# Kernel tuning notes

Hardware: AMD Instinct MI355X
Metric: run time of the kernel (lower is better)

Reference implementation:

```python
import jax, jax.numpy as jnp
import numpy as np
import math

B, S, D = 4, 4096, 1024
H = 16
HD = D // H          # head_dim = 64
M = 256              # nb_features (random projection dim)


def _orthogonal_gaussian(key, m, d):
    # FAVOR+ orthogonal random features: blocks of d orthogonal rows,
    # each row rescaled to a chi-distributed norm (norm of a d-dim gaussian).
    n_blocks = int(math.ceil(m / d))
    keys = jax.random.split(key, n_blocks + 1)
    blocks = []
    for i in range(n_blocks):
        g = jax.random.normal(keys[i], (d, d), dtype=jnp.float32)
        q, _ = jnp.linalg.qr(g)
        blocks.append(q.T)
    W = jnp.concatenate(blocks, axis=0)[:m]  # [m, d]
    norms = jnp.linalg.norm(
        jax.random.normal(keys[-1], (m, d), dtype=jnp.float32), axis=1, keepdims=True)
    return W * norms


def _softmax_kernel(x, proj, is_query, eps=1e-4):
    # x: [b,h,s,d]; proj: [m,d]. Standard FAVOR+ positive softmax features.
    d = x.shape[-1]
    ratio = proj.shape[0] ** -0.5
    x = x * (d ** -0.25)
    u = jnp.einsum('bhsd,md->bhsm', x, proj)  # projection
    diag = 0.5 * jnp.sum(x * x, axis=-1, keepdims=True)  # [b,h,s,1]
    if is_query:
        stab = jnp.max(u, axis=-1, keepdims=True)
    else:
        stab = jnp.max(u, axis=(-1, -2), keepdims=True)
    return ratio * (jnp.exp(u - diag - stab) + eps)


def performer_attention(Q, K, V, mask, proj):
    # Q,K,V: [b,h,s,d], mask: [b,s]
    scale = HD ** -0.25
    m4 = mask[:, None, :, None]
    Qs = Q * scale
    Ks = K * scale * m4
    Vs = V * m4
    q_prime = _softmax_kernel(Qs, proj, is_query=True)   # [b,h,s,m]
    k_prime = _softmax_kernel(Ks, proj, is_query=False)  # [b,h,s,m]
    # linear attention: O(s*m*d)
    kv = jnp.einsum('bhsm,bhsd->bhmd', k_prime, Vs)      # [b,h,m,d]
    z = 1.0 / (jnp.einsum('bhsm,bhm->bhs', q_prime, jnp.sum(k_prime, axis=2)) + 1e-6)
    out = jnp.einsum('bhsm,bhmd->bhsd', q_prime, kv) * z[..., None]
    return out


def setup_inputs() -> dict:
    key = jax.random.key(0)
    ks = jax.random.split(key, 9)
    X = jax.random.normal(ks[0], (B, S, D), dtype=jnp.float32)
    mask = jnp.ones((B, S), dtype=jnp.float32)
    s = D ** -0.5
    Wq = jax.random.normal(ks[1], (D, D), dtype=jnp.float32) * s
    bq = jnp.zeros((D,), dtype=jnp.float32)
    Wk = jax.random.normal(ks[2], (D, D), dtype=jnp.float32) * s
    bk = jnp.zeros((D,), dtype=jnp.float32)
    Wv = jax.random.normal(ks[3], (D, D), dtype=jnp.float32) * s
    bv = jnp.zeros((D,), dtype=jnp.float32)
    proj = _orthogonal_gaussian(ks[4], M, HD)
    return {"X": X, "mask": mask, "Wq": Wq, "bq": bq, "Wk": Wk, "bk": bk,
            "Wv": Wv, "bv": bv, "proj": proj}


def _split_heads(x):
    b, s, _ = x.shape
    return x.reshape(b, s, H, HD).transpose(0, 2, 1, 3)


def reference(X, mask, Wq, bq, Wk, bk, Wv, bv, proj):
    Q = _split_heads(X @ Wq + bq)
    K = _split_heads(X @ Wk + bk)
    V = _split_heads(X @ Wv + bv)
    attn = performer_attention(Q, K, V, mask, proj)  # [b,h,s,hd]
    out = attn.transpose(0, 2, 1, 3).reshape(B, S, D)
    return out
```

## Files before the change

### kernel.cpp

```cpp
#include <hip/hip_runtime.h>
#include <stdint.h>

#define DEVI static __device__ __forceinline__

typedef unsigned short u16;
typedef unsigned int u32;
typedef __attribute__((ext_vector_type(8))) short short8;
typedef __attribute__((ext_vector_type(4))) float f32x4;
typedef __attribute__((ext_vector_type(4))) unsigned short ushort4_t;

#define BB 4
#define SS 4096
#define DD 1024
#define HH 16
#define HDD 64
#define MM 256
#define BHN 64

DEVI u16 f2bf(float f) {
    u32 u = __float_as_uint(f);
    u += 0x7fffu + ((u >> 16) & 1u);
    return (u16)(u >> 16);
}
DEVI float bf2f(u16 h) { return __uint_as_float(((u32)h) << 16); }

typedef __attribute__((address_space(1))) const unsigned int as1_u32;
typedef __attribute__((address_space(3))) unsigned int as3_u32;
DEVI void load_lds16(const void* g, void* lds) {
    __builtin_amdgcn_global_load_lds((as1_u32*)g, (as3_u32*)lds, 16, 0, 0);
}


__global__ void conv_bf16(const float* __restrict__ src, u16* __restrict__ dst, int n4) {
    int i = blockIdx.x * 256 + threadIdx.x;
    if (i < n4) {
        float4 v = reinterpret_cast<const float4*>(src)[i];
        ushort4_t o = { f2bf(v.x), f2bf(v.y), f2bf(v.z), f2bf(v.w) };
        reinterpret_cast<ushort4_t*>(dst)[i] = o;
    }
}

__global__ void conv_w(const float* __restrict__ Wq, const float* __restrict__ Wk,
                       const float* __restrict__ Wv, u16* __restrict__ Wt) {
    __shared__ float tile[64][65];
    const int jt = blockIdx.x, kt = blockIdx.y;
    const float* src = (jt < 16) ? Wq : (jt < 32) ? Wk : Wv;
    const int j0 = (jt & 15) * 64, k0 = kt * 64;
    const int t = threadIdx.x;
    for (int i = 0; i < 16; ++i) {
        int lin = t + i * 256;
        int kl = lin >> 6, jl = lin & 63;
        tile[kl][jl] = src[(size_t)(k0 + kl) * DD + j0 + jl];
    }
    __syncthreads();
    const int jg0 = jt * 64;
    for (int i = 0; i < 16; ++i) {
        int lin = t + i * 256;
        int jl = lin >> 6, kl = lin & 63;
        Wt[(size_t)(jg0 + jl) * DD + k0 + kl] = f2bf(tile[kl][jl]);
    }
}

__global__ __launch_bounds__(512, 2) void gemm1_m8(
    const u16* __restrict__ Xbf, const u16* __restrict__ Wt,
    const float* __restrict__ bq, const float* __restrict__ bk, const float* __restrict__ bv,
    const float* __restrict__ mask,
    u16* __restrict__ Qh, u16* __restrict__ Kh, u16* __restrict__ Vt,
    float* __restrict__ dq, float* __restrict__ dk)
{
    extern __shared__ __align__(16) char smem[];
    const int tid = threadIdx.x, l = tid & 63, wv = tid >> 6;
    const int wm = wv >> 2, wn = wv & 3;
    const int bid = blockIdx.x;
    const int xcd = bid & 7, i6 = bid >> 3;
    const int bx = xcd * 8 + i6 / 12, by = i6 % 12;
    const int row0 = bx * 256, col0 = by * 256;

    const int srow = tid >> 3;
    const int scol = ((tid & 7) ^ (srow & 7)) * 8;

    #define ABUF(p) ((char*)smem + (p) * 32768)
    #define BBUF(p) ((char*)smem + 65536 + (p) * 32768)
    #define STA(p, kt, r) load_lds16(Xbf + (size_t)(row0 + (r)*64 + srow) * DD + (kt)*64 + scol, \
                                     ABUF(p) + (r)*8192 + wv*1024)
    #define STB(p, kt, r) load_lds16(Wt + (size_t)(col0 + (r)*64 + srow) * DD + (kt)*64 + scol, \
                                     BBUF(p) + (r)*8192 + wv*1024)

    STA(0,0,0); STA(0,0,1); STA(0,0,2); STA(0,0,3);
    STB(0,0,0); STB(0,0,1); STB(0,0,2); STB(0,0,3);
    STA(1,1,0); STA(1,1,1); STA(1,1,2); STA(1,1,3);
    asm volatile("s_waitcnt vmcnt(4)" ::: "memory");
    __builtin_amdgcn_s_barrier();
    __builtin_amdgcn_sched_barrier(0);

    f32x4 acc[8][4] = {};
    const int arow_b = wm * 128 + (l & 15);
    const int brow_b = wn * 64 + (l & 15);
    const int cb_b = (l >> 4) * 16;
    const int lx = (l & 7) << 4;

    for (int kt = 0; kt < 16; ++kt) {
        const int p = kt & 1, pn = p ^ 1;
        const bool haveN = (kt + 1) < 16;
        short8 bfr[2][2];
#pragma unroll
        for (int ph = 0; ph < 4; ++ph) {
            const int mh = ph & 1, nh = ph >> 1;
            if (haveN) STB(pn, kt + 1, ph);
            if (mh == 0) {
#pragma unroll
                for (int j = 0; j < 2; ++j) {
                    const int br = brow_b + (nh * 2 + j) * 16;
#pragma unroll
                    for (int ks = 0; ks < 2; ++ks)
                        bfr[j][ks] = *(const short8*)(BBUF(p) + br * 128 + ((cb_b + ks * 64) ^ lx));
                }
            }
            short8 a[4][2];
#pragma unroll
            for (int i = 0; i < 4; ++i) {
                const int ar = arow_b + (mh * 4 + i) * 16;
#pragma unroll
                for (int ks = 0; ks < 2; ++ks)
                    a[i][ks] = *(const short8*)(ABUF(p) + ar * 128 + ((cb_b + ks * 64) ^ lx));
            }
            __builtin_amdgcn_s_barrier();
            asm volatile("s_waitcnt lgkmcnt(0)" ::: "memory");
            __builtin_amdgcn_sched_barrier(0);
            __builtin_amdgcn_s_setprio(1);
#pragma unroll
            for (int i = 0; i < 4; ++i)
#pragma unroll
                for (int j = 0; j < 2; ++j) {
                    acc[mh*4+i][nh*2+j] = __builtin_amdgcn_mfma_f32_16x16x32_bf16(a[i][0], bfr[j][0], acc[mh*4+i][nh*2+j], 0, 0, 0);
                    acc[mh*4+i][nh*2+j] = __builtin_amdgcn_mfma_f32_16x16x32_bf16(a[i][1], bfr[j][1], acc[mh*4+i][nh*2+j], 0, 0, 0);
                }
            __builtin_amdgcn_s_setprio(0);
            __builtin_amdgcn_sched_barrier(0);
            __builtin_amdgcn_s_barrier();
        }
        if (kt + 2 < 16) {
            STA(p, kt + 2, 0); STA(p, kt + 2, 1); STA(p, kt + 2, 2); STA(p, kt + 2, 3);
            asm volatile("s_waitcnt vmcnt(4)" ::: "memory");
        } else {
            asm volatile("s_waitcnt vmcnt(0)" ::: "memory");
        }
        __builtin_amdgcn_s_barrier();
        __builtin_amdgcn_sched_barrier(0);
    }

    const int region = by >> 2;
    const int h = ((by & 3) << 2) + wn;
    const int rg = row0 + wm * 128;
    const int b = rg >> 12;
    const int sb = rg & 4095;
    const size_t bh = (size_t)(b * HH + h);
    const int dd = l & 15;
    const int jbase = ((by & 3) << 8) + wn * 64;

    if (region == 0) {
        float bias[4];
#pragma unroll
        for (int nf = 0; nf < 4; ++nf) bias[nf] = bq[jbase + nf * 16 + dd];
#pragma unroll
        for (int mf = 0; mf < 8; ++mf) {
            float ds4[4];
#pragma unroll
            for (int g = 0; g < 4; ++g) {
                const int s = sb + mf * 16 + ((l >> 4) << 2) + g;
                float dsum = 0.f;
#pragma unroll
                for (int nf = 0; nf < 4; ++nf) {
                    u16 hv = f2bf((acc[mf][nf][g] + bias[nf]) * 0.125f);
                    Qh[(bh * SS + s) * HDD + nf * 16 + dd] = hv;
                    float fv = bf2f(hv);
                    dsum += fv * fv;
                }
                dsum += __shfl_xor(dsum, 1);
                dsum += __shfl_xor(dsum, 2);
                dsum += __shfl_xor(dsum, 4);
                dsum += __shfl_xor(dsum, 8);
                ds4[g] = 0.5f * dsum;
            }
            if (dd == 0)
                *(float4*)(dq + bh * SS + sb + mf * 16 + ((l >> 4) << 2)) =
                    make_float4(ds4[0], ds4[1], ds4[2], ds4[3]);
        }
    } else if (region == 1) {
        float bias[4];
#pragma unroll
        for (int nf = 0; nf < 4; ++nf) bias[nf] = bk[jbase + nf * 16 + dd];
#pragma unroll
        for (int mf = 0; mf < 8; ++mf) {
            float ds4[4];
#pragma unroll
            for (int g = 0; g < 4; ++g) {
                const int s = sb + mf * 16 + ((l >> 4) << 2) + g;
                const float m = mask[b * SS + s];
                float dsum = 0.f;
#pragma unroll
                for (int nf = 0; nf < 4; ++nf) {
                    u16 hv = f2bf((acc[mf][nf][g] + bias[nf]) * m * 0.125f);
                    Kh[(bh * SS + s) * HDD + nf * 16 + dd] = hv;
                    float fv = bf2f(hv);
                    dsum += fv * fv;
                }
                dsum += __shfl_xor(dsum, 1);
                dsum += __shfl_xor(dsum, 2);
                dsum += __shfl_xor(dsum, 4);
                dsum += __shfl_xor(dsum, 8);
                ds4[g] = 0.5f * dsum;
            }
            if (dd == 0)
                *(float4*)(dk + bh * SS + sb + mf * 16 + ((l >> 4) << 2)) =
                    make_float4(ds4[0], ds4[1], ds4[2], ds4[3]);
        }
    } else {
        float bias[4];
#pragma unroll
        for (int nf = 0; nf < 4; ++nf) bias[nf] = bv[jbase + nf * 16 + dd];
#pragma unroll
        for (int mf = 0; mf < 8; ++mf) {
            const int s0 = sb + mf * 16 + ((l >> 4) << 2);
#pragma unroll
            for (int nf = 0; nf < 4; ++nf) {
                ushort4_t pk;
#pragma unroll
                for (int g = 0; g < 4; ++g) {
                    const float m = mask[b * SS + s0 + g];
                    pk[g] = f2bf((acc[mf][nf][g] + bias[nf]) * m);
                }
                *(ushort4_t*)(Vt + (bh * HDD + nf * 16 + dd) * SS + s0) = pk;
            }
        }
    }
    #undef ABUF
    #undef BBUF
    #undef STA
    #undef STB
}

__global__ __launch_bounds__(256, 2) void kv_fused(
    const u16* __restrict__ Kh, const u16* __restrict__ Vt,
    const u16* __restrict__ projb, const float* __restrict__ dk,
    float* __restrict__ kv_part, float* __restrict__ ksum_part,
    float* __restrict__ vsum_part, float* __restrict__ lstab)
{
    extern __shared__ __align__(16) char ksm[];
    #define KLDS(b) ((char*)ksm + (b) * 8192)
    #define VLDS(b) ((char*)ksm + 24576 + (b) * 8192)
    u16* Kp = (u16*)((char*)ksm + 49152);
    const int tid = threadIdx.x, l = tid & 63, wv = tid >> 6;
    const int ck = blockIdx.x, bh = blockIdx.y;
    short8 pb[4][2];
#pragma unroll
    for (int nf = 0; nf < 4; ++nf)
#pragma unroll
        for (int ks = 0; ks < 2; ++ks)
            pb[nf][ks] = *(const short8*)(projb + (wv * 64 + nf * 16 + (l & 15)) * HDD + ks * 32 + (l >> 4) * 8);
    const size_t sbase = (size_t)bh * SS + ck * 512;

    #define KSTAGE(buf, it8) do { \
        const int s0_ = (it8) * 64; \
        _Pragma("unroll") \
        for (int c = 0; c < 2; ++c) { \
            const int rb = wv * 16 + c * 8; \
            const int r = rb + (l >> 3); \
            const int sc = ((l & 7) ^ (r & 7)) * 8; \
            load_lds16(Kh + (sbase + s0_ + r) * HDD + sc, KLDS(buf) + rb * 128); \
        } \
    } while (0)
    #define VSTAGE(buf, it8) do { \
        const int s0_ = (it8) * 64; \
        _Pragma("unroll") \
        for (int c = 0; c < 2; ++c) { \
            const int rb = wv * 16 + c * 8; \
            const int r = rb + (l >> 3); \
            const int sc = ((l & 7) ^ (r & 7)) * 8; \
            load_lds16(Vt + ((size_t)bh * HDD + r) * SS + ck * 512 + s0_ + sc, VLDS(buf) + rb * 128); \
        } \
    } while (0)

    float mrun = -3.0e38f;
    f32x4 acc[4][4] = {};
    float ksc[4] = {0.f, 0.f, 0.f, 0.f};
    float vsc[4] = {0.f, 0.f, 0.f, 0.f};
    KSTAGE(0, 0); VSTAGE(0, 0);
    for (int it = 0; it < 8; ++it) {
        if (it + 1 < 8) {
            KSTAGE((it + 1) % 3, it + 1);
            VSTAGE((it + 1) % 3, it + 1);
            asm volatile("s_waitcnt vmcnt(4)" ::: "memory");
        } else {
            asm volatile("s_waitcnt vmcnt(0)" ::: "memory");
        }
        __syncthreads();
        const int bs = it % 3;
        const int s0 = it * 64;
        f32x4 u4[4][4];
#pragma unroll
        for (int sf = 0; sf < 4; ++sf) {
#pragma unroll
            for (int nf = 0; nf < 4; ++nf) u4[sf][nf] = (f32x4){0.f, 0.f, 0.f, 0.f};
            const int s = sf * 16 + (l & 15);
#pragma unroll
            for (int ks = 0; ks < 2; ++ks) {
                short8 ak = *(const short8*)(KLDS(bs) + s * 128 + ((ks * 64 + (l >> 4) * 16) ^ ((s & 7) << 4)));
#pragma unroll
                for (int nf = 0; nf < 4; ++nf)
                    u4[sf][nf] = __builtin_amdgcn_mfma_f32_16x16x32_bf16(ak, pb[nf][ks], u4[sf][nf], 0, 0, 0);
            }
        }
        float pmax = -3.0e38f;
#pragma unroll
        for (int sf = 0; sf < 4; ++sf)
#pragma unroll
            for (int nf = 0; nf < 4; ++nf)
#pragma unroll
                for (int g = 0; g < 4; ++g) pmax = fmaxf(pmax, u4[sf][nf][g]);
#pragma unroll
        for (int o = 1; o < 64; o <<= 1) pmax = fmaxf(pmax, __shfl_xor(pmax, o));
        if (pmax > mrun) {
            const float fac = __expf(mrun - pmax);
            mrun = pmax;
#pragma unroll
            for (int mf = 0; mf < 4; ++mf)
#pragma unroll
                for (int nf = 0; nf < 4; ++nf)
#pragma unroll
                    for (int g = 0; g < 4; ++g) acc[mf][nf][g] *= fac;
#pragma unroll
            for (int nf = 0; nf < 4; ++nf) ksc[nf] *= fac;
        }
#pragma unroll
        for (int sf = 0; sf < 4; ++sf) {
            const int srow = sf * 16 + (l >> 4) * 4;
            const float4 dkv = *(const float4*)(dk + sbase + s0 + srow);
#pragma unroll
            for (int nf = 0; nf < 4; ++nf) {
                const int m = wv * 64 + nf * 16 + (l & 15);
                u16 h0 = f2bf(__expf(u4[sf][nf][0] - dkv.x - mrun));
                u16 h1 = f2bf(__expf(u4[sf][nf][1] - dkv.y - mrun));
                u16 h2 = f2bf(__expf(u4[sf][nf][2] - dkv.z - mrun));
                u16 h3 = f2bf(__expf(u4[sf][nf][3] - dkv.w - mrun));
                ksc[nf] += bf2f(h0) + bf2f(h1) + bf2f(h2) + bf2f(h3);
                uint2 w; w.x = (u32)h0 | ((u32)h1 << 16); w.y = (u32)h2 | ((u32)h3 << 16);
                *(uint2*)((char*)Kp + m * 128 + ((srow * 2) ^ ((m & 7) << 4))) = w;
            }
        }
        __syncthreads();
#pragma unroll
        for (int ks = 0; ks < 2; ++ks) {
            short8 am[4], bv8[4];
#pragma unroll
            for (int mf = 0; mf < 4; ++mf) {
                const int m = wv * 64 + mf * 16 + (l & 15);
                am[mf] = *(const short8*)((const char*)Kp + m * 128 + ((ks * 64 + (l >> 4) * 16) ^ ((m & 7) << 4)));
            }
#pragma unroll
            for (int nf = 0; nf < 4; ++nf) {
                const int d = nf * 16 + (l & 15);
                bv8[nf] = *(const short8*)(VLDS(bs) + d * 128 + ((ks * 64 + (l >> 4) * 16) ^ ((d & 7) << 4)));
                float vs = 0.f;
#pragma unroll
                for (int e = 0; e < 8; ++e) vs += bf2f((u16)bv8[nf][e]);
                vsc[nf] += vs;
            }
#pragma unroll
            for (int mf = 0; mf < 4; ++mf)
#pragma unroll
                for (int nf = 0; nf < 4; ++nf)
                    acc[mf][nf] = __builtin_amdgcn_mfma_f32_16x16x32_bf16(am[mf], bv8[nf], acc[mf][nf], 0, 0, 0);
        }
    }
    if (l == 0) lstab[((size_t)ck * BHN + bh) * 4 + wv] = mrun;
    const size_t pbase = (size_t)ck * BHN + bh;
#pragma unroll
    for (int nf = 0; nf < 4; ++nf) {
        float v = ksc[nf];
        v += __shfl_xor(v, 16);
        v += __shfl_xor(v, 32);
        if (l < 16) ksum_part[pbase * MM + wv * 64 + nf * 16 + l] = v;
        float w = vsc[nf];
        w += __shfl_xor(w, 16);
        w += __shfl_xor(w, 32);
        if (wv == 0 && l < 16) vsum_part[pbase * HDD + nf * 16 + l] = w;
    }
#pragma unroll
    for (int mf = 0; mf < 4; ++mf)
#pragma unroll
        for (int nf = 0; nf < 4; ++nf)
            *(f32x4*)(kv_part + (pbase * HDD + nf * 16 + (l & 15)) * MM + wv * 64 + mf * 16 + (l >> 4) * 4) = acc[mf][nf];
    #undef KLDS
    #undef VLDS
    #undef KSTAGE
    #undef VSTAGE
}

__global__ void reduceB3(const float* __restrict__ kv_part, const float* __restrict__ ksum_part,
                         const float* __restrict__ vsum_part, const float* __restrict__ lstab,
                         u16* __restrict__ Bmat) {
    __shared__ float f[8][4];
    const int bh = blockIdx.x, n = blockIdx.y, t = threadIdx.x;
    if (t < 32) {
        float lv = lstab[((size_t)(t >> 2) * BHN + bh) * 4 + (t & 3)];
        float g = lv;
#pragma unroll
        for (int o = 1; o < 32; o <<= 1) g = fmaxf(g, __shfl_xor(g, o));
        f[t >> 2][t & 3] = __expf(lv - g);
    }
    __syncthreads();
    const int grp = t >> 6;
    float s = 0.f;
    if (n < 64) {
        float vsg = 0.f;
#pragma unroll
        for (int ck = 0; ck < 8; ++ck) {
            vsg += vsum_part[((size_t)ck * BHN + bh) * HDD + n];
            s += kv_part[(((size_t)ck * BHN + bh) * HDD + n) * MM + t] * f[ck][grp];
        }
        s = 0.0625f * (s + 1e-4f * vsg);
    } else if (n == 64) {
#pragma unroll
        for (int ck = 0; ck < 8; ++ck)
            s += ksum_part[((size_t)ck * BHN + bh) * MM + t] * f[ck][grp];
        s = 0.0625f * (s + 1e-4f * 4096.0f);
    }
    Bmat[((size_t)bh * 80 + n) * MM + t] = (n <= 64) ? f2bf(s) : (u16)0;
}

__global__ __launch_bounds__(256) void out_fused(
    const u16* __restrict__ Qh, const u16* __restrict__ projb,
    const float* __restrict__ dq, const u16* __restrict__ Bmat,
    float* __restrict__ out)
{
    __shared__ __align__(16) u16 Qlds[64 * 64];
    __shared__ __align__(16) u16 qlds[64 * 256];
    __shared__ float red[4][64];
    const int tid = threadIdx.x, l = tid & 63, wv = tid >> 6;
    const int rt = blockIdx.x, bh = blockIdx.y;
    const size_t srowbase = (size_t)bh * SS + rt * 64;
#pragma unroll
    for (int c = 0; c < 2; ++c) {
        const int rb = wv * 16 + c * 8;
        const int r = rb + (l >> 3);
        load_lds16(Qh + (srowbase + r) * HDD + (((l & 7) ^ (r & 7)) * 8), (char*)Qlds + rb * 128);
    }
    short8 pa[4][2];
#pragma unroll
    for (int mf = 0; mf < 4; ++mf)
#pragma unroll
        for (int ks = 0; ks < 2; ++ks)
            pa[mf][ks] = *(const short8*)(projb + (wv * 64 + mf * 16 + (l & 15)) * HDD + ks * 32 + (l >> 4) * 8);
    __syncthreads();
    f32x4 u[4][4] = {};
#pragma unroll
    for (int ks = 0; ks < 2; ++ks) {
        short8 bq8[4];
#pragma unroll
        for (int nf = 0; nf < 4; ++nf) {
            const int s = nf * 16 + (l & 15);
            bq8[nf] = *(const short8*)((const char*)Qlds + s * 128 + ((ks * 64 + (l >> 4) * 16) ^ ((s & 7) << 4)));
        }
#pragma unroll
        for (int mf = 0; mf < 4; ++mf)
#pragma unroll
            for (int nf = 0; nf < 4; ++nf)
                u[mf][nf] = __builtin_amdgcn_mfma_f32_16x16x32_bf16(pa[mf][ks], bq8[nf], u[mf][nf], 0, 0, 0);
    }
#pragma unroll
    for (int nf = 0; nf < 4; ++nf) {
        float v = -3.0e38f;
#pragma unroll
        for (int mf = 0; mf < 4; ++mf)
#pragma unroll
            for (int g = 0; g < 4; ++g) v = fmaxf(v, u[mf][nf][g]);
        v = fmaxf(v, __shfl_xor(v, 16));
        v = fmaxf(v, __shfl_xor(v, 32));
        if ((l >> 4) == 0) red[wv][nf * 16 + l] = v;
    }
    __syncthreads();
#pragma unroll
    for (int nf = 0; nf < 4; ++nf) {
        const int s = nf * 16 + (l & 15);
        const float mx = fmaxf(fmaxf(red[0][s], red[1][s]), fmaxf(red[2][s], red[3][s]));
        const float dg = dq[srowbase + s];
#pragma unroll
        for (int mf = 0; mf < 4; ++mf) {
            u16 h0 = f2bf(0.0625f * (__expf(u[mf][nf][0] - dg - mx) + 1e-4f));
            u16 h1 = f2bf(0.0625f * (__expf(u[mf][nf][1] - dg - mx) + 1e-4f));
            u16 h2 = f2bf(0.0625f * (__expf(u[mf][nf][2] - dg - mx) + 1e-4f));
            u16 h3 = f2bf(0.0625f * (__expf(u[mf][nf][3] - dg - mx) + 1e-4f));
            uint2 w; w.x = (u32)h0 | ((u32)h1 << 16); w.y = (u32)h2 | ((u32)h3 << 16);
            const int mb = (wv * 64 + mf * 16 + (l >> 4) * 4) * 2;
            *(uint2*)((char*)qlds + s * 512 + (mb ^ ((s & 7) << 4))) = w;
        }
    }
    __syncthreads();
    const u16* bbase = Bmat + (size_t)bh * 20480;
    f32x4 acc[4][2] = {};
#pragma unroll
    for (int kt = 0; kt < 8; ++kt) {
        short8 aq[4], bb[2];
#pragma unroll
        for (int mf = 0; mf < 4; ++mf) {
            const int s = mf * 16 + (l & 15);
            aq[mf] = *(const short8*)((const char*)qlds + s * 512 + ((kt * 64 + (l >> 4) * 16) ^ ((s & 7) << 4)));
        }
        bb[0] = *(const short8*)(bbase + (wv * 16 + (l & 15)) * 256 + kt * 32 + (l >> 4) * 8);
        bb[1] = *(const short8*)(bbase + (64 + (l & 15)) * 256 + kt * 32 + (l >> 4) * 8);
#pragma unroll
        for (int mf = 0; mf < 4; ++mf)
#pragma unroll
            for (int nf = 0; nf < 2; ++nf)
                acc[mf][nf] = __builtin_amdgcn_mfma_f32_16x16x32_bf16(aq[mf], bb[nf], acc[mf][nf], 0, 0, 0);
    }
    const int b = bh >> 4, h = bh & 15;
#pragma unroll
    for (int mf = 0; mf < 4; ++mf) {
#pragma unroll
        for (int g = 0; g < 4; ++g) {
            const float den = __shfl(acc[mf][1][g], (l & 48));
            const float z = 1.0f / (den + 1e-6f);
            const int s = rt * 64 + mf * 16 + (l >> 4) * 4 + g;
            out[((size_t)b * SS + s) * DD + h * HDD + wv * 16 + (l & 15)] = acc[mf][0][g] * z;
        }
    }
}

extern "C" void kernel_launch(void* const* d_in, const int* in_sizes, int n_in,
                              void* d_out, int out_size, void* d_ws, size_t ws_size,
                              hipStream_t stream)
{
    const float* X    = (const float*)d_in[0];
    const float* mask = (const float*)d_in[1];
    const float* Wq   = (const float*)d_in[2];
    const float* bq   = (const float*)d_in[3];
    const float* Wk   = (const float*)d_in[4];
    const float* bk   = (const float*)d_in[5];
    const float* Wv   = (const float*)d_in[6];
    const float* bv   = (const float*)d_in[7];
    const float* proj = (const float*)d_in[8];
    float* out = (float*)d_out;

    char* p = (char*)d_ws;
    u16* Xbf = (u16*)p;
    float* kv_part = (float*)p; p += 33554432;
    u16* Wt = (u16*)p;    p += 6291456;
    u16* projb = (u16*)p; p += 32768;
    u16* Qh = (u16*)p;    p += 33554432;
    u16* Kh = (u16*)p;    p += 33554432;
    u16* Vt = (u16*)p;    p += 33554432;
    float* dq = (float*)p; p += 1048576;
    float* dk = (float*)p; p += 1048576;
    float* ksum_part = (float*)p; p += 524288;
    u16* Bmat = (u16*)p;  p += 2621440;
    float* vsum_part = (float*)p; p += 131072;
    float* lstab = (float*)p; p += 8192;
    if (ws_size < 145924096ull) return;

    hipFuncSetAttribute((const void*)gemm1_m8, hipFuncAttributeMaxDynamicSharedMemorySize, 131072);
    hipFuncSetAttribute((const void*)kv_fused, hipFuncAttributeMaxDynamicSharedMemorySize, 81920);

    conv_bf16<<<16384, 256, 0, stream>>>(X, Xbf, 4194304);
    conv_w<<<dim3(48, 16), 256, 0, stream>>>(Wq, Wk, Wv, Wt);
    conv_bf16<<<16, 256, 0, stream>>>(proj, projb, 4096);
    gemm1_m8<<<768, 512, 131072, stream>>>(Xbf, Wt, bq, bk, bv, mask, Qh, Kh, Vt, dq, dk);
    kv_fused<<<dim3(8, 64), 256, 81920, stream>>>(Kh, Vt, projb, dk, kv_part, ksum_part, vsum_part, lstab);
    reduceB3<<<dim3(64, 80), 256, 0, stream>>>(kv_part, ksum_part, vsum_part, lstab, Bmat);
    out_fused<<<dim3(64, 64), 256, 0, stream>>>(Qh, projb, dq, Bmat, out);
}
```

Measured before the change: 268.8 us.

## Halve GEMM K-tile to 32 with new LDS swizzle to double occupancy

Reworks the QKV projection GEMM to use a K step of 32 instead of 64, halving the LDS footprint from 128KB to 64KB and raising the launch bound to allow more resident blocks. The LDS layout and swizzle are redone so two 32-wide rows share a 128-byte line, and the pipeline becomes a simple double buffer with one barrier per K step instead of per-phase barriers. This is meant to improve latency hiding through occupancy, at the cost of twice as many loop iterations and waiting on all loads each step (vmcnt(0)). With 512 threads and 128 accumulator floats per thread, register pressure may cap actual occupancy.

```diff
diff --git a/kernel.cpp b/kernel.cpp
--- a/kernel.cpp
+++ b/kernel.cpp
@@ -61,7 +61,7 @@
     }
 }
 
-__global__ __launch_bounds__(512, 2) void gemm1_m8(
+__global__ __launch_bounds__(512, 4) void gemm1_bk32(
     const u16* __restrict__ Xbf, const u16* __restrict__ Wt,
     const float* __restrict__ bq, const float* __restrict__ bk, const float* __restrict__ bv,
     const float* __restrict__ mask,
@@ -76,75 +76,66 @@
     const int bx = xcd * 8 + i6 / 12, by = i6 % 12;
     const int row0 = bx * 256, col0 = by * 256;
 
-    const int srow = tid >> 3;
-    const int scol = ((tid & 7) ^ (srow & 7)) * 8;
-
-    #define ABUF(p) ((char*)smem + (p) * 32768)
-    #define BBUF(p) ((char*)smem + 65536 + (p) * 32768)
-    #define STA(p, kt, r) load_lds16(Xbf + (size_t)(row0 + (r)*64 + srow) * DD + (kt)*64 + scol, \
-                                     ABUF(p) + (r)*8192 + wv*1024)
-    #define STB(p, kt, r) load_lds16(Wt + (size_t)(col0 + (r)*64 + srow) * DD + (kt)*64 + scol, \
-                                     BBUF(p) + (r)*8192 + wv*1024)
-
-    STA(0,0,0); STA(0,0,1); STA(0,0,2); STA(0,0,3);
-    STB(0,0,0); STB(0,0,1); STB(0,0,2); STB(0,0,3);
-    STA(1,1,0); STA(1,1,1); STA(1,1,2); STA(1,1,3);
-    asm volatile("s_waitcnt vmcnt(4)" ::: "memory");
+    int sA[2];
+#pragma unroll
+    for (int j = 0; j < 2; ++j) {
+        const int o = j * 8192 + tid * 16;
+        const int R = o >> 7;
+        const int logpos = (o & 127) ^ ((R & 7) << 4);
+        const int r = 2 * R + (logpos >> 6);
+        const int c8 = (logpos >> 4) & 3;
+        sA[j] = r * DD + c8 * 8;
+    }
+    const size_t xbase = (size_t)row0 * DD;
+    const size_t wbase = (size_t)col0 * DD;
+
+    #define ABUF(b) ((char*)smem + (b) * 16384)
+    #define BBUF(b) ((char*)smem + 32768 + (b) * 16384)
+    #define STA(b, kt, j) load_lds16(Xbf + xbase + (kt) * 32 + sA[j], ABUF(b) + (j) * 8192 + wv * 1024)
+    #define STB(b, kt, j) load_lds16(Wt + wbase + (kt) * 32 + sA[j], BBUF(b) + (j) * 8192 + wv * 1024)
+
+    STA(0, 0, 0); STA(0, 0, 1); STB(0, 0, 0); STB(0, 0, 1);
+    asm volatile("s_waitcnt vmcnt(0)" ::: "memory");
     __builtin_amdgcn_s_barrier();
     __builtin_amdgcn_sched_barrier(0);
 
     f32x4 acc[8][4] = {};
-    const int arow_b = wm * 128 + (l & 15);
-    const int brow_b = wn * 64 + (l & 15);
-    const int cb_b = (l >> 4) * 16;
-    const int lx = (l & 7) << 4;
-
-    for (int kt = 0; kt < 16; ++kt) {
+    const int hl = (l & 15) >> 1;
+    const int xorc = hl << 4;
+    const int pa = ((wm * 64 + hl) * 128 + (l & 1) * 64 + (l >> 4) * 16) ^ xorc;
+    const int pb = ((wn * 32 + hl) * 128 + (l & 1) * 64 + (l >> 4) * 16) ^ xorc;
+
+    for (int kt = 0; kt < 32; ++kt) {
         const int p = kt & 1, pn = p ^ 1;
-        const bool haveN = (kt + 1) < 16;
-        short8 bfr[2][2];
-#pragma unroll
-        for (int ph = 0; ph < 4; ++ph) {
-            const int mh = ph & 1, nh = ph >> 1;
-            if (haveN) STB(pn, kt + 1, ph);
-            if (mh == 0) {
-#pragma unroll
-                for (int j = 0; j < 2; ++j) {
-                    const int br = brow_b + (nh * 2 + j) * 16;
-#pragma unroll
-                    for (int ks = 0; ks < 2; ++ks)
-                        bfr[j][ks] = *(const short8*)(BBUF(p) + br * 128 + ((cb_b + ks * 64) ^ lx));
-                }
-            }
-            short8 a[4][2];
-#pragma unroll
-            for (int i = 0; i < 4; ++i) {
-                const int ar = arow_b + (mh * 4 + i) * 16;
-#pragma unroll
-                for (int ks = 0; ks < 2; ++ks)
-                    a[i][ks] = *(const short8*)(ABUF(p) + ar * 128 + ((cb_b + ks * 64) ^ lx));
-            }
-            __builtin_amdgcn_s_barrier();
-            asm volatile("s_waitcnt lgkmcnt(0)" ::: "memory");
-            __builtin_amdgcn_sched_barrier(0);
+        const bool more = (kt + 1) < 32;
+        short8 bfr[4];
+#pragma unroll
+        for (int q = 0; q < 4; ++q) {
+            if (more) {
+                if (q == 0)      STA(pn, kt + 1, 0);
+                else if (q == 1) STA(pn, kt + 1, 1);
+                else if (q == 2) STB(pn, kt + 1, 0);
+                else             STB(pn, kt + 1, 1);
+            }
+            if (q == 0) {
+#pragma unroll
+                for (int nf = 0; nf < 4; ++nf)
+                    bfr[nf] = *(const short8*)(BBUF(p) + pb + nf * 1024);
+            }
+            short8 a[2];
+#pragma unroll
+            for (int i = 0; i < 2; ++i)
+                a[i] = *(const short8*)(ABUF(p) + pa + (q * 2 + i) * 1024);
             __builtin_amdgcn_s_setprio(1);
 #pragma unroll
-            for (int i = 0; i < 4; ++i)
-#pragma unroll
-                for (int j = 0; j < 2; ++j) {
-                    acc[mh*4+i][nh*2+j] = __builtin_amdgcn_mfma_f32_16x16x32_bf16(a[i][0], bfr[j][0], acc[mh*4+i][nh*2+j], 0, 0, 0);
-                    acc[mh*4+i][nh*2+j] = __builtin_amdgcn_mfma_f32_16x16x32_bf16(a[i][1], bfr[j][1], acc[mh*4+i][nh*2+j], 0, 0, 0);
-                }
+            for (int i = 0; i < 2; ++i)
+#pragma unroll
+                for (int nf = 0; nf < 4; ++nf)
+                    acc[q * 2 + i][nf] = __builtin_amdgcn_mfma_f32_16x16x32_bf16(a[i], bfr[nf], acc[q * 2 + i][nf], 0, 0, 0);
             __builtin_amdgcn_s_setprio(0);
             __builtin_amdgcn_sched_barrier(0);
-            __builtin_amdgcn_s_barrier();
-        }
-        if (kt + 2 < 16) {
-            STA(p, kt + 2, 0); STA(p, kt + 2, 1); STA(p, kt + 2, 2); STA(p, kt + 2, 3);
-            asm volatile("s_waitcnt vmcnt(4)" ::: "memory");
-        } else {
-            asm volatile("s_waitcnt vmcnt(0)" ::: "memory");
-        }
+        }
+        asm volatile("s_waitcnt vmcnt(0)" ::: "memory");
         __builtin_amdgcn_s_barrier();
         __builtin_amdgcn_sched_barrier(0);
     }
@@ -559,13 +550,13 @@
     float* lstab = (float*)p; p += 8192;
     if (ws_size < 145924096ull) return;
 
-    hipFuncSetAttribute((const void*)gemm1_m8, hipFuncAttributeMaxDynamicSharedMemorySize, 131072);
+    hipFuncSetAttribute((const void*)gemm1_bk32, hipFuncAttributeMaxDynamicSharedMemorySize, 65536);
     hipFuncSetAttribute((const void*)kv_fused, hipFuncAttributeMaxDynamicSharedMemorySize, 81920);
 
     conv_bf16<<<16384, 256, 0, stream>>>(X, Xbf, 4194304);
     conv_w<<<dim3(48, 16), 256, 0, stream>>>(Wq, Wk, Wv, Wt);
     conv_bf16<<<16, 256, 0, stream>>>(proj, projb, 4096);
-    gemm1_m8<<<768, 512, 131072, stream>>>(Xbf, Wt, bq, bk, bv, mask, Qh, Kh, Vt, dq, dk);
+    gemm1_bk32<<<768, 512, 65536, stream>>>(Xbf, Wt, bq, bk, bv, mask, Qh, Kh, Vt, dq, dk);
     kv_fused<<<dim3(8, 64), 256, 81920, stream>>>(Kh, Vt, projb, dk, kv_part, ksum_part, vsum_part, lstab);
     reduceB3<<<dim3(64, 80), 256, 0, stream>>>(kv_part, ksum_part, vsum_part, lstab, Bmat);
     out_fused<<<dim3(64, 64), 256, 0, stream>>>(Qh, projb, dq, Bmat, out);
```

New measurement: 1.014 ms. 277% more time.
